# Optimization experiments

Hardware: AMD Instinct MI355X
Metric: run time of the kernel (lower is better)

Reference implementation:

```python
import jax, jax.numpy as jnp
import numpy as np

T, D = 4096, 2048
H, DK, DV = 6, 256, 512        # heads, head_k_dim, head_v_dim (expand_v=2)
KD, VD = H * DK, H * DV        # 1536, 3072
KSZ = 4                        # conv_size
GEN = D // 8                   # generator reduction 8 -> 256
EPS = 1e-5                     # norm_eps


def setup_inputs() -> dict:
    key = jax.random.key(0)
    ks = jax.random.split(key, 12)
    std = 0.02
    p = lambda i, shape: jax.random.normal(ks[i], shape, jnp.float32) * std
    rng = np.random.default_rng(0)
    A = rng.uniform(0.0, 16.0, H).astype(np.float32)
    dt = np.exp(rng.uniform(0, 1, H) * (np.log(0.1) - np.log(0.001)) + np.log(0.001)).astype(np.float32)
    dt = np.clip(dt, 1e-4, None)
    inv_dt = (dt + np.log(-np.expm1(-dt))).astype(np.float32)
    return {
        'hidden_states': jax.random.normal(ks[0], (T, D), jnp.float32),
        'Wq': p(1, (D, KD)), 'Wk': p(2, (D, KD)), 'Wv': p(3, (D, VD)),
        'Wb': p(4, (D, H)), 'Wa': p(5, (D, H)), 'Wg': p(6, (D, VD)), 'Wo': p(7, (VD, D)),
        'A_log': jnp.asarray(np.log(A)), 'dt_bias': jnp.asarray(inv_dt),
        'conv_w': p(8, (VD, KSZ)), 'gen_w1': p(9, (D, GEN)), 'gen_w2': p(10, (GEN, KSZ)),
        'norm_w': jnp.ones((DV,), jnp.float32),
    }


def _l2norm(x):
    return x * jax.lax.rsqrt(jnp.sum(x * x, -1, keepdims=True) + 1e-6)


def reference(hidden_states, Wq, Wk, Wv, Wb, Wa, Wg, Wo, A_log, dt_bias, conv_w, gen_w1, gen_w2, norm_w):
    h = hidden_states[None]                             # [1,T,D]
    q = jax.nn.silu(h @ Wq)                             # [1,T,KD]
    k = jax.nn.silu(h @ Wk)
    x = h @ Wv                                          # [1,T,VD]
    # dynamic short convolution: per-token kernel added to static depthwise kernel
    dyn = jax.nn.silu(h @ gen_w1) @ gen_w2              # [1,T,KSZ]
    xpad = jnp.pad(x, ((0, 0), (KSZ - 1, 0), (0, 0)))   # causal padding
    v = jnp.zeros_like(x)
    for j in range(KSZ):
        v = v + (conv_w[None, None, :, j] + dyn[:, :, None, j]) * xpad[:, j:j + x.shape[1], :]
    v = jax.nn.silu(v)

    B = 1
    q = _l2norm(q.reshape(B, -1, H, DK))                # use_qk_l2norm_in_kernel=True
    k = _l2norm(k.reshape(B, -1, H, DK))
    v = v.reshape(B, -1, H, DV)
    beta = jax.nn.sigmoid(h @ Wb)                       # [1,T,H]
    g = -jnp.exp(A_log) * jax.nn.softplus(h @ Wa + dt_bias)  # [1,T,H] decay log-gates
    scale = DK ** -0.5

    def step(S, inp):                                   # gated delta rule recurrence
        qt, kt, vt, gt, bt = inp
        S = S * jnp.exp(gt)[..., None, None]            # [B,H,DK,DV]
        dv = (vt - jnp.einsum('bhk,bhkv->bhv', kt, S)) * bt[..., None]
        S = S + kt[..., :, None] * dv[..., None, :]
        ot = jnp.einsum('bhk,bhkv->bhv', qt, S) * scale
        return S, ot

    S0 = jnp.zeros((B, H, DK, DV), jnp.float32)
    tm = lambda a: jnp.moveaxis(a, 1, 0)                # time-major for scan
    _, o = jax.lax.scan(step, S0, (tm(q), tm(k), tm(v), tm(g), tm(beta)))
    o = jnp.moveaxis(o, 0, 1)                           # [1,T,H,DV]

    gate = (h @ Wg).reshape(B, -1, H, DV)
    rms = jax.lax.rsqrt(jnp.mean(o * o, -1, keepdims=True) + EPS)
    o = o * rms * norm_w * jax.nn.silu(gate)            # gated RMSNorm
    o = o.reshape(B, -1, VD) @ Wo                       # [1,T,D]
    return o[0]
```

## Files before the change

### kernel.cpp

```cpp
#include <hip/hip_runtime.h>
#include <hip/hip_bf16.h>
#include <math.h>

#define T_LEN 4096
#define DIM   2048
#define NH    6
#define DK    256
#define DVh   512
#define KD    1536
#define VD    3072
#define CK    64
#define NCHK  (T_LEN / CK)

typedef __attribute__((ext_vector_type(8))) short bf16x8;
typedef __attribute__((ext_vector_type(4))) float f32x4;

__device__ __forceinline__ float silu_f(float v){ return v / (1.f + __expf(-v)); }

__device__ __forceinline__ unsigned short f2bf(float f) {
  unsigned int u = __float_as_uint(f);
  unsigned int r = u + 0x7FFFu + ((u >> 16) & 1u);
  return (unsigned short)(r >> 16);
}
__device__ __forceinline__ float bf2f(unsigned short s) {
  return __uint_as_float(((unsigned int)s) << 16);
}

__device__ __forceinline__ void bar_lds() {
  __builtin_amdgcn_sched_barrier(0);
  asm volatile("s_waitcnt lgkmcnt(0)" ::: "memory");
  __builtin_amdgcn_s_barrier();
  __builtin_amdgcn_sched_barrier(0);
}

__global__ __launch_bounds__(256) void cast_bf16(
    const float* __restrict__ in, unsigned short* __restrict__ out)
{
  int i = blockIdx.x * 256 + threadIdx.x;
  float4 v4 = ((const float4*)in)[i];
  ushort4 o4;
  o4.x = f2bf(v4.x); o4.y = f2bf(v4.y); o4.z = f2bf(v4.z); o4.w = f2bf(v4.w);
  ((ushort4*)out)[i] = o4;
}

__global__ __launch_bounds__(256) void tcast(
    const float* __restrict__ in, unsigned short* __restrict__ out, int R, int Cn)
{
  __shared__ float tile[32][33];
  int bx = blockIdx.x * 32;
  int by = blockIdx.y * 32;
  int tx = threadIdx.x & 31, ty = threadIdx.x >> 5;
#pragma unroll
  for (int i = 0; i < 32; i += 8)
    tile[ty + i][tx] = in[(size_t)(by + ty + i) * Cn + bx + tx];
  __syncthreads();
#pragma unroll
  for (int i = 0; i < 32; i += 8)
    out[(size_t)(bx + ty + i) * R + by + tx] = f2bf(tile[tx][ty + i]);
}

__global__ __launch_bounds__(256) void gemm_bt_bf16(
    const unsigned short* __restrict__ A, const unsigned short* __restrict__ BT,
    void* __restrict__ Cout, int M, int N, int K, int act)
{
  __shared__ unsigned short As[128 * 32];
  __shared__ unsigned short Bs[128 * 32];
  const int tid = threadIdx.x;
  const int bm = blockIdx.y * 128, bn = blockIdx.x * 128;
  const int lane = tid & 63, wave = tid >> 6;
  const int wm = (wave >> 1) * 64, wn = (wave & 1) * 64;
  const int fr = lane & 15, kq = lane >> 4;

  f32x4 acc[4][4];
#pragma unroll
  for (int i = 0; i < 4; ++i)
#pragma unroll
    for (int j = 0; j < 4; ++j) acc[i][j] = (f32x4){0.f, 0.f, 0.f, 0.f};

  const int r0 = tid >> 2, c0 = (tid & 3) * 8;
  const int r1 = r0 + 64;

  for (int k0 = 0; k0 < K; k0 += 32) {
    __builtin_amdgcn_global_load_lds(
        (const __attribute__((address_space(1))) unsigned int*)(A + (size_t)(bm + r0) * K + k0 + c0),
        (__attribute__((address_space(3))) unsigned int*)(As + r0 * 32 + c0), 16, 0, 0);
    __builtin_amdgcn_global_load_lds(
        (const __attribute__((address_space(1))) unsigned int*)(A + (size_t)(bm + r1) * K + k0 + c0),
        (__attribute__((address_space(3))) unsigned int*)(As + r1 * 32 + c0), 16, 0, 0);
    __builtin_amdgcn_global_load_lds(
        (const __attribute__((address_space(1))) unsigned int*)(BT + (size_t)(bn + r0) * K + k0 + c0),
        (__attribute__((address_space(3))) unsigned int*)(Bs + r0 * 32 + c0), 16, 0, 0);
    __builtin_amdgcn_global_load_lds(
        (const __attribute__((address_space(1))) unsigned int*)(BT + (size_t)(bn + r1) * K + k0 + c0),
        (__attribute__((address_space(3))) unsigned int*)(Bs + r1 * 32 + c0), 16, 0, 0);
    __syncthreads();

    bf16x8 af[4], bfr[4];
#pragma unroll
    for (int i = 0; i < 4; ++i)
      af[i] = *(const bf16x8*)(As + (wm + i * 16 + fr) * 32 + kq * 8);
#pragma unroll
    for (int j = 0; j < 4; ++j)
      bfr[j] = *(const bf16x8*)(Bs + (wn + j * 16 + fr) * 32 + kq * 8);
#pragma unroll
    for (int i = 0; i < 4; ++i)
#pragma unroll
      for (int j = 0; j < 4; ++j)
        acc[i][j] = __builtin_amdgcn_mfma_f32_16x16x32_bf16(af[i], bfr[j], acc[i][j], 0, 0, 0);
    __syncthreads();
  }

  if (act == 2) {
    unsigned short* C = (unsigned short*)Cout;
#pragma unroll
    for (int i = 0; i < 4; ++i) {
      int rbase = bm + wm + i * 16 + kq * 4;
#pragma unroll
      for (int r = 0; r < 4; ++r) {
        size_t rowoff = (size_t)(rbase + r) * N + bn + wn + fr;
#pragma unroll
        for (int j = 0; j < 4; ++j) C[rowoff + j * 16] = f2bf(acc[i][j][r]);
      }
    }
  } else {
    float* C = (float*)Cout;
#pragma unroll
    for (int i = 0; i < 4; ++i) {
      int rbase = bm + wm + i * 16 + kq * 4;
#pragma unroll
      for (int r = 0; r < 4; ++r) {
        size_t rowoff = (size_t)(rbase + r) * N + bn + wn + fr;
#pragma unroll
        for (int j = 0; j < 4; ++j) {
          float v = acc[i][j][r];
          if (act == 1) v = silu_f(v);
          C[rowoff + j * 16] = v;
        }
      }
    }
  }
}

__global__ __launch_bounds__(256) void proj_dyn(
    const float* __restrict__ tg, const float* __restrict__ w2, float* __restrict__ dyn)
{
  int t = blockIdx.x, tid = threadIdx.x;
  float g = tg[(size_t)t * 256 + tid];
  float p[4];
#pragma unroll
  for (int j = 0; j < 4; ++j) p[j] = g * w2[tid * 4 + j];
#pragma unroll
  for (int j = 0; j < 4; ++j)
    for (int m = 32; m >= 1; m >>= 1) p[j] += __shfl_xor(p[j], m);
  __shared__ float red[4][4];
  if ((tid & 63) == 0) {
    int w = tid >> 6;
#pragma unroll
    for (int j = 0; j < 4; ++j) red[w][j] = p[j];
  }
  __syncthreads();
  if (tid < 4) dyn[(size_t)t * 4 + tid] = red[0][tid] + red[1][tid] + red[2][tid] + red[3][tid];
}

__global__ __launch_bounds__(256) void proj_bg(
    const float* __restrict__ h, const float* __restrict__ Wb, const float* __restrict__ Wa,
    const float* __restrict__ A_log, const float* __restrict__ dt_bias,
    float* __restrict__ beta, float* __restrict__ gout)
{
  int t = blockIdx.x, tid = threadIdx.x;
  float pb[6], pa[6];
#pragma unroll
  for (int j = 0; j < 6; ++j) { pb[j] = 0.f; pa[j] = 0.f; }
  for (int d = tid; d < DIM; d += 256) {
    float hv = h[(size_t)t * DIM + d];
#pragma unroll
    for (int j = 0; j < 6; ++j) {
      pb[j] += hv * Wb[d * 6 + j];
      pa[j] += hv * Wa[d * 6 + j];
    }
  }
#pragma unroll
  for (int j = 0; j < 6; ++j)
    for (int m = 32; m >= 1; m >>= 1) { pb[j] += __shfl_xor(pb[j], m); pa[j] += __shfl_xor(pa[j], m); }
  __shared__ float rb[4][6], ra[4][6];
  if ((tid & 63) == 0) {
    int w = tid >> 6;
#pragma unroll
    for (int j = 0; j < 6; ++j) { rb[w][j] = pb[j]; ra[w][j] = pa[j]; }
  }
  __syncthreads();
  if (tid < 6) {
    int j = tid;
    float sb = rb[0][j] + rb[1][j] + rb[2][j] + rb[3][j];
    float sa = ra[0][j] + ra[1][j] + ra[2][j] + ra[3][j];
    beta[(size_t)t * 6 + j] = 1.f / (1.f + expf(-sb));
    float z = sa + dt_bias[j];
    float sp = (z > 20.f) ? z : log1pf(expf(z));
    gout[(size_t)t * 6 + j] = -expf(A_log[j]) * sp;
  }
}

__global__ __launch_bounds__(256) void conv_kernel(
    const float* __restrict__ x, const float* __restrict__ dyn,
    const float* __restrict__ cw, float* __restrict__ v)
{
  int c = blockIdx.x * 256 + threadIdx.x;
  int t = blockIdx.y;
  float4 w4 = ((const float4*)cw)[c];
  float d0 = dyn[t * 4 + 0], d1 = dyn[t * 4 + 1], d2 = dyn[t * 4 + 2], d3 = dyn[t * 4 + 3];
  float acc = (w4.w + d3) * x[(size_t)t * VD + c];
  if (t >= 1) acc += (w4.z + d2) * x[(size_t)(t - 1) * VD + c];
  if (t >= 2) acc += (w4.y + d1) * x[(size_t)(t - 2) * VD + c];
  if (t >= 3) acc += (w4.x + d0) * x[(size_t)(t - 3) * VD + c];
  v[(size_t)t * VD + c] = silu_f(acc);
}

__global__ __launch_bounds__(64) void l2norm_qk(
    float* __restrict__ q, float* __restrict__ k)
{
  size_t base = (size_t)blockIdx.x * 256;
  int tid = threadIdx.x;
  float4 qv = ((float4*)(q + base))[tid];
  float4 kv = ((float4*)(k + base))[tid];
  float sq = qv.x*qv.x + qv.y*qv.y + qv.z*qv.z + qv.w*qv.w;
  float sk = kv.x*kv.x + kv.y*kv.y + kv.z*kv.z + kv.w*kv.w;
  for (int m = 32; m >= 1; m >>= 1) { sq += __shfl_xor(sq, m); sk += __shfl_xor(sk, m); }
  float rq = rsqrtf(sq + 1e-6f) * 0.0625f;
  float rk = rsqrtf(sk + 1e-6f);
  qv.x *= rq; qv.y *= rq; qv.z *= rq; qv.w *= rq;
  kv.x *= rk; kv.y *= rk; kv.z *= rk; kv.w *= rk;
  ((float4*)(q + base))[tid] = qv;
  ((float4*)(k + base))[tid] = kv;
}

__global__ __launch_bounds__(64) void cumsum_g(
    const float* __restrict__ g, float* __restrict__ c, float* __restrict__ gammas)
{
  int ch = blockIdx.x, h = blockIdx.y;
  int t0 = ch * CK;
  int lane = threadIdx.x;
  float cum = g[(size_t)(t0 + lane) * 6 + h];
  for (int off = 1; off < 64; off <<= 1) {
    float n = __shfl_up(cum, off);
    if (lane >= off) cum += n;
  }
  c[(size_t)h * T_LEN + t0 + lane] = cum;
  if (lane == 63) gammas[h * NCHK + ch] = __expf(cum);
}

__global__ __launch_bounds__(384) void scale_kq(
    const float* __restrict__ q, const float* __restrict__ k, const float* __restrict__ c,
    unsigned short* __restrict__ Qb, unsigned short* __restrict__ Kb)
{
  int t = blockIdx.x;
  int tid = threadIdx.x;
  int h = tid >> 6;
  float w1 = __expf(c[(size_t)h * T_LEN + t]);
  size_t off = (size_t)t * KD + tid * 4;
  float4 qv = *(const float4*)(q + off);
  float4 kv = *(const float4*)(k + off);
  ushort4 qo, ko;
  qo.x = f2bf(w1 * qv.x); qo.y = f2bf(w1 * qv.y); qo.z = f2bf(w1 * qv.z); qo.w = f2bf(w1 * qv.w);
  ko.x = f2bf(w1 * kv.x); ko.y = f2bf(w1 * kv.y); ko.z = f2bf(w1 * kv.z); ko.w = f2bf(w1 * kv.w);
  *(ushort4*)(Qb + off) = qo;
  *(ushort4*)(Kb + off) = ko;
}

__global__ __launch_bounds__(256) void make_khT(
    const float* __restrict__ k, const float* __restrict__ c,
    unsigned short* __restrict__ KhT)
{
  int ch = blockIdx.x, h = blockIdx.y;
  int t0 = ch * CK;
  int tt = threadIdx.x & 63, ks = threadIdx.x >> 6;
  float cend = c[(size_t)h * T_LEN + t0 + 63];
  float w2 = __expf(cend - c[(size_t)h * T_LEN + t0 + tt]);
  size_t obase = ((size_t)(h * NCHK + ch)) * DK * CK;
#pragma unroll 8
  for (int kb2 = 0; kb2 < 64; ++kb2) {
    int kk = ks * 64 + kb2;
    float kv = k[(size_t)(t0 + tt) * KD + h * 256 + kk];
    KhT[obase + (size_t)kk * CK + tt] = f2bf(w2 * kv);
  }
}

__global__ __launch_bounds__(256) void chunk_lp(
    const float* __restrict__ q, const float* __restrict__ k,
    const float* __restrict__ c, const float* __restrict__ beta,
    float* __restrict__ Lg, unsigned short* __restrict__ Pm)
{
  const int ch = blockIdx.x, h = blockIdx.y;
  const int t0 = ch * CK;
  const int tid = threadIdx.x;
  const int w = tid >> 6, lane = tid & 63, fr = lane & 15, kq = lane >> 4;
  __shared__ unsigned short kb[64][264];
  __shared__ unsigned short qb[64][264];
  __shared__ float cs[64], bs[64];
#pragma unroll
  for (int i = 0; i < 16; ++i) {
    int fi = tid + i * 256;
    int r = fi >> 6, d4 = fi & 63;
    float4 kv = *(const float4*)(k + (size_t)(t0 + r) * KD + h * 256 + d4 * 4);
    float4 qv = *(const float4*)(q + (size_t)(t0 + r) * KD + h * 256 + d4 * 4);
    ushort4 k4, q4;
    k4.x = f2bf(kv.x); k4.y = f2bf(kv.y); k4.z = f2bf(kv.z); k4.w = f2bf(kv.w);
    q4.x = f2bf(qv.x); q4.y = f2bf(qv.y); q4.z = f2bf(qv.z); q4.w = f2bf(qv.w);
    *(ushort4*)&kb[r][d4 * 4] = k4;
    *(ushort4*)&qb[r][d4 * 4] = q4;
  }
  if (tid < 64) {
    cs[tid] = c[(size_t)h * T_LEN + t0 + tid];
    bs[tid] = beta[(size_t)(t0 + tid) * 6 + h];
  }
  __syncthreads();

  f32x4 akk[4], aqk[4];
#pragma unroll
  for (int j = 0; j < 4; ++j) { akk[j] = (f32x4){0,0,0,0}; aqk[j] = (f32x4){0,0,0,0}; }
#pragma unroll
  for (int kt = 0; kt < 8; ++kt) {
    bf16x8 ak = *(const bf16x8*)&kb[16 * w + fr][kt * 32 + kq * 8];
    bf16x8 aq = *(const bf16x8*)&qb[16 * w + fr][kt * 32 + kq * 8];
#pragma unroll
    for (int j = 0; j < 4; ++j) {
      bf16x8 b = *(const bf16x8*)&kb[j * 16 + fr][kt * 32 + kq * 8];
      akk[j] = __builtin_amdgcn_mfma_f32_16x16x32_bf16(ak, b, akk[j], 0, 0, 0);
      aqk[j] = __builtin_amdgcn_mfma_f32_16x16x32_bf16(aq, b, aqk[j], 0, 0, 0);
    }
  }
  size_t base = ((size_t)(h * NCHK + ch)) * CK * CK;
#pragma unroll
  for (int j = 0; j < 4; ++j) {
#pragma unroll
    for (int r = 0; r < 4; ++r) {
      int t = 16 * w + kq * 4 + r, col = j * 16 + fr;
      float e = __expf(fminf(cs[t] - cs[col], 0.f));
      Lg[base + t * 64 + col] = (col < t) ? bs[t] * e * akk[j][r] : 0.f;
      Pm[base + t * 64 + col] = f2bf((col <= t) ? e * aqk[j][r] : 0.f);
    }
  }
}

__global__ __launch_bounds__(64) void tri_inv(
    const float* __restrict__ Lg, const float* __restrict__ beta,
    unsigned short* __restrict__ Tm)
{
  const int ch = blockIdx.x, h = blockIdx.y;
  const size_t base = ((size_t)(h * NCHK + ch)) * CK * CK;
  const int j = threadIdx.x;
  __shared__ float Ll[64][65];
  __shared__ float Tl[64][65];
  for (int t = 0; t < 64; ++t) Ll[t][j] = Lg[base + t * 64 + j];
  __syncthreads();
  for (int t = 0; t < 64; ++t) {
    float s;
    if (j > t) s = 0.f;
    else if (j == t) s = 1.f;
    else {
      s = 0.f;
      for (int m = j; m < t; ++m) s -= Ll[t][m] * Tl[m][j];
    }
    Tl[t][j] = s;
  }
  float bj = beta[(size_t)(ch * 64 + j) * 6 + h];
  for (int t = 0; t < 64; ++t) Tm[base + t * 64 + j] = f2bf(Tl[t][j] * bj);
}

__global__ __launch_bounds__(256) void scan_chunk(
    const unsigned short* __restrict__ Kb,
    const unsigned short* __restrict__ Qb,
    const unsigned short* __restrict__ KhT,
    const unsigned short* __restrict__ Tm,
    const unsigned short* __restrict__ Pm,
    const float* __restrict__ gammas,
    float* __restrict__ VO)
{
  const int h = blockIdx.y, sl = blockIdx.x;
  const int tid = threadIdx.x;
  const int w = tid >> 6, lane = tid & 63;
  const int fr = lane & 15, kq = lane >> 4;

  __shared__ unsigned short S0h[16][264];
  __shared__ unsigned short S0l[16][264];
  __shared__ unsigned short XT[16][72];
  __shared__ unsigned short DVT[16][72];

  f32x4 st[4];
#pragma unroll
  for (int i = 0; i < 4; ++i) st[i] = (f32x4){0.f, 0.f, 0.f, 0.f};

  const int colg = h * DVh + sl * 16 + fr;
  const size_t hc0 = (size_t)h * NCHK;

  bf16x8 kfA[8], kfB[8];
  float vlA[4], vlB[4];

#define PREF_KV(KF, VL, chn) do { \
    const unsigned short* krow_ = Kb + (size_t)((chn) * CK + 16 * w + fr) * KD + h * 256 + kq * 8; \
    _Pragma("unroll") \
    for (int kt = 0; kt < 8; ++kt) KF[kt] = *(const bf16x8*)(krow_ + kt * 32); \
    _Pragma("unroll") \
    for (int r = 0; r < 4; ++r) VL[r] = VO[(size_t)((chn) * CK + 16 * w + kq * 4 + r) * VD + colg]; \
  } while (0)

#define CHUNK_BODY(chx, KF, VL, KFN, VLN) do { \
    const int ch_ = (chx); \
    const int t0_ = ch_ * CK; \
    const size_t cb_ = hc0 + ch_; \
     \
    bf16x8 qf[8]; \
    { const unsigned short* qrow_ = Qb + (size_t)(t0_ + 16 * w + fr) * KD + h * 256 + kq * 8; \
      _Pragma("unroll") \
      for (int kt = 0; kt < 8; ++kt) qf[kt] = *(const bf16x8*)(qrow_ + kt * 32); } \
    bf16x8 tf[2], pf[2]; \
    { const unsigned short* trow_ = Tm + (cb_ * CK + 16 * w + fr) * CK + kq * 8; \
      const unsigned short* prow_ = Pm + (cb_ * CK + 16 * w + fr) * CK + kq * 8; \
      tf[0] = *(const bf16x8*)(trow_); tf[1] = *(const bf16x8*)(trow_ + 32); \
      pf[0] = *(const bf16x8*)(prow_); pf[1] = *(const bf16x8*)(prow_ + 32); } \
    bf16x8 hfr[4][2]; \
    _Pragma("unroll") \
    for (int i = 0; i < 4; ++i) { \
      const unsigned short* hrow_ = KhT + (cb_ * DK + 64 * w + 16 * i + fr) * CK + kq * 8; \
      hfr[i][0] = *(const bf16x8*)(hrow_); hfr[i][1] = *(const bf16x8*)(hrow_ + 32); } \
    const float gam_ = gammas[cb_]; \
     \
    _Pragma("unroll") \
    for (int i = 0; i < 4; ++i) { \
      ushort4 hi4, lo4; \
      float s0 = st[i][0], s1 = st[i][1], s2 = st[i][2], s3 = st[i][3]; \
      hi4.x = f2bf(s0); lo4.x = f2bf(s0 - bf2f(hi4.x)); \
      hi4.y = f2bf(s1); lo4.y = f2bf(s1 - bf2f(hi4.y)); \
      hi4.z = f2bf(s2); lo4.z = f2bf(s2 - bf2f(hi4.z)); \
      hi4.w = f2bf(s3); lo4.w = f2bf(s3 - bf2f(hi4.w)); \
      *(ushort4*)&S0h[fr][64 * w + 16 * i + kq * 4] = hi4; \
      *(ushort4*)&S0l[fr][64 * w + 16 * i + kq * 4] = lo4; } \
     \
    { const int chn_ = (ch_ + 1 < NCHK) ? ch_ + 1 : ch_; PREF_KV(KFN, VLN, chn_); } \
    bar_lds(); \
     \
    { f32x4 yh = (f32x4){0.f,0.f,0.f,0.f}, yl = (f32x4){0.f,0.f,0.f,0.f}; \
      _Pragma("unroll") \
      for (int kt = 0; kt < 8; ++kt) { \
        bf16x8 bh_ = *(const bf16x8*)&S0h[fr][kt * 32 + kq * 8]; \
        bf16x8 bl_ = *(const bf16x8*)&S0l[fr][kt * 32 + kq * 8]; \
        yh = __builtin_amdgcn_mfma_f32_16x16x32_bf16(KF[kt], bh_, yh, 0, 0, 0); \
        yl = __builtin_amdgcn_mfma_f32_16x16x32_bf16(KF[kt], bl_, yl, 0, 0, 0); } \
      ushort4 x4; \
      x4.x = f2bf(VL[0] - (yh[0] + yl[0])); \
      x4.y = f2bf(VL[1] - (yh[1] + yl[1])); \
      x4.z = f2bf(VL[2] - (yh[2] + yl[2])); \
      x4.w = f2bf(VL[3] - (yh[3] + yl[3])); \
      *(ushort4*)&XT[fr][16 * w + kq * 4] = x4; } \
    bar_lds(); \
     \
    { f32x4 d = (f32x4){0.f,0.f,0.f,0.f}; \
      _Pragma("unroll") \
      for (int kt = 0; kt < 2; ++kt) { \
        bf16x8 b_ = *(const bf16x8*)&XT[fr][kt * 32 + kq * 8]; \
        d = __builtin_amdgcn_mfma_f32_16x16x32_bf16(tf[kt], b_, d, 0, 0, 0); } \
      ushort4 d4; \
      d4.x = f2bf(d[0]); d4.y = f2bf(d[1]); d4.z = f2bf(d[2]); d4.w = f2bf(d[3]); \
      *(ushort4*)&DVT[fr][16 * w + kq * 4] = d4; } \
    bar_lds(); \
     \
    { f32x4 oh = (f32x4){0.f,0.f,0.f,0.f}, ol = (f32x4){0.f,0.f,0.f,0.f}, op = (f32x4){0.f,0.f,0.f,0.f}; \
      _Pragma("unroll") \
      for (int kt = 0; kt < 8; ++kt) { \
        bf16x8 bh_ = *(const bf16x8*)&S0h[fr][kt * 32 + kq * 8]; \
        bf16x8 bl_ = *(const bf16x8*)&S0l[fr][kt * 32 + kq * 8]; \
        oh = __builtin_amdgcn_mfma_f32_16x16x32_bf16(qf[kt], bh_, oh, 0, 0, 0); \
        ol = __builtin_amdgcn_mfma_f32_16x16x32_bf16(qf[kt], bl_, ol, 0, 0, 0); } \
      _Pragma("unroll") \
      for (int kt = 0; kt < 2; ++kt) { \
        bf16x8 b_ = *(const bf16x8*)&DVT[fr][kt * 32 + kq * 8]; \
        op = __builtin_amdgcn_mfma_f32_16x16x32_bf16(pf[kt], b_, op, 0, 0, 0); } \
      _Pragma("unroll") \
      for (int r = 0; r < 4; ++r) \
        VO[(size_t)(t0_ + 16 * w + kq * 4 + r) * VD + colg] = oh[r] + ol[r] + op[r]; } \
     \
    _Pragma("unroll") \
    for (int i = 0; i < 4; ++i) { \
      st[i][0] *= gam_; st[i][1] *= gam_; st[i][2] *= gam_; st[i][3] *= gam_; \
      _Pragma("unroll") \
      for (int kt = 0; kt < 2; ++kt) { \
        bf16x8 b_ = *(const bf16x8*)&DVT[fr][kt * 32 + kq * 8]; \
        st[i] = __builtin_amdgcn_mfma_f32_16x16x32_bf16(hfr[i][kt], b_, st[i], 0, 0, 0); } } \
    bar_lds(); \
  } while (0)

  PREF_KV(kfA, vlA, 0);
  for (int ch = 0; ch < NCHK; ch += 2) {
    CHUNK_BODY(ch,     kfA, vlA, kfB, vlB);
    CHUNK_BODY(ch + 1, kfB, vlB, kfA, vlA);
  }
#undef CHUNK_BODY
#undef PREF_KV
}

__global__ __launch_bounds__(256) void norm_gate(
    const float* __restrict__ o, const unsigned short* __restrict__ gate,
    const float* __restrict__ nw, unsigned short* __restrict__ out)
{
  int th = blockIdx.x, tid = threadIdx.x;
  size_t base = (size_t)th * DVh;
  float x0 = o[base + tid], x1 = o[base + 256 + tid];
  float ss = x0 * x0 + x1 * x1;
  for (int m = 32; m >= 1; m >>= 1) ss += __shfl_xor(ss, m);
  __shared__ float red[4];
  if ((tid & 63) == 0) red[tid >> 6] = ss;
  __syncthreads();
  float rms = rsqrtf((red[0] + red[1] + red[2] + red[3]) * (1.f / 512.f) + 1e-5f);
  float g0 = bf2f(gate[base + tid]), g1 = bf2f(gate[base + 256 + tid]);
  out[base + tid]       = f2bf(x0 * rms * nw[tid]       * silu_f(g0));
  out[base + 256 + tid] = f2bf(x1 * rms * nw[tid + 256] * silu_f(g1));
}

extern "C" void kernel_launch(void* const* d_in, const int* in_sizes, int n_in,
                              void* d_out, int out_size, void* d_ws, size_t ws_size,
                              hipStream_t stream)
{
  const float* h       = (const float*)d_in[0];
  const float* Wq      = (const float*)d_in[1];
  const float* Wk      = (const float*)d_in[2];
  const float* Wv      = (const float*)d_in[3];
  const float* Wb      = (const float*)d_in[4];
  const float* Wa      = (const float*)d_in[5];
  const float* Wg      = (const float*)d_in[6];
  const float* Wo      = (const float*)d_in[7];
  const float* A_log   = (const float*)d_in[8];
  const float* dt_bias = (const float*)d_in[9];
  const float* conv_w  = (const float*)d_in[10];
  const float* gen_w1  = (const float*)d_in[11];
  const float* gen_w2  = (const float*)d_in[12];
  const float* norm_w  = (const float*)d_in[13];
  float* out = (float*)d_out;

  const size_t TK = (size_t)T_LEN * KD, TV = (size_t)T_LEN * VD, TD = (size_t)T_LEN * DIM;

  float* ws   = (float*)d_ws;
  float* q    = ws;
  float* k    = q    + TK;
  float* x    = k    + TK;
  float* v    = x    + TV;
  float* tg   = v    + TV;
  float* dyn  = tg   + (size_t)T_LEN * 256;
  float* beta = dyn  + (size_t)T_LEN * 4;
  float* g    = beta + (size_t)T_LEN * 6;
  float* c    = g    + (size_t)T_LEN * 6;
  float* gam  = c    + (size_t)NH * T_LEN;
  float* fend = gam  + 512;
  unsigned short* bh      = (unsigned short*)fend;
  unsigned short* wT      = bh      + TD;
  unsigned short* gate_bf = wT      + (size_t)DIM * VD;
  unsigned short* go_bf   = gate_bf + TV;
  unsigned short* Kb_s  = bh;
  unsigned short* Qb_s  = (unsigned short*)x;
  unsigned short* KhT_s = Qb_s + TK;
  unsigned short* Tm_s  = KhT_s + TK;
  unsigned short* Pm_s  = Tm_s + (size_t)NH * NCHK * CK * CK;
  float* Lg = (float*)go_bf;

  dim3 blk(256);
  cast_bf16<<<(TD / 4) / 256, blk, 0, stream>>>(h, bh);
  tcast<<<dim3(KD / 32, DIM / 32), blk, 0, stream>>>(Wq, wT, DIM, KD);
  gemm_bt_bf16<<<dim3(KD / 128, T_LEN / 128), blk, 0, stream>>>(bh, wT, q, T_LEN, KD, DIM, 1);
  tcast<<<dim3(KD / 32, DIM / 32), blk, 0, stream>>>(Wk, wT, DIM, KD);
  gemm_bt_bf16<<<dim3(KD / 128, T_LEN / 128), blk, 0, stream>>>(bh, wT, k, T_LEN, KD, DIM, 1);
  tcast<<<dim3(VD / 32, DIM / 32), blk, 0, stream>>>(Wv, wT, DIM, VD);
  gemm_bt_bf16<<<dim3(VD / 128, T_LEN / 128), blk, 0, stream>>>(bh, wT, x, T_LEN, VD, DIM, 0);
  tcast<<<dim3(VD / 32, DIM / 32), blk, 0, stream>>>(Wg, wT, DIM, VD);
  gemm_bt_bf16<<<dim3(VD / 128, T_LEN / 128), blk, 0, stream>>>(bh, wT, gate_bf, T_LEN, VD, DIM, 2);
  tcast<<<dim3(256 / 32, DIM / 32), blk, 0, stream>>>(gen_w1, wT, DIM, 256);
  gemm_bt_bf16<<<dim3(256 / 128, T_LEN / 128), blk, 0, stream>>>(bh, wT, tg, T_LEN, 256, DIM, 1);

  proj_dyn<<<T_LEN, blk, 0, stream>>>(tg, gen_w2, dyn);
  proj_bg<<<T_LEN, blk, 0, stream>>>(h, Wb, Wa, A_log, dt_bias, beta, g);
  conv_kernel<<<dim3(VD / 256, T_LEN), blk, 0, stream>>>(x, dyn, conv_w, v);
  l2norm_qk<<<T_LEN * NH, 64, 0, stream>>>(q, k);

  cumsum_g<<<dim3(NCHK, NH), 64, 0, stream>>>(g, c, gam);
  scale_kq<<<T_LEN, 384, 0, stream>>>(q, k, c, Qb_s, Kb_s);
  make_khT<<<dim3(NCHK, NH), blk, 0, stream>>>(k, c, KhT_s);
  chunk_lp<<<dim3(NCHK, NH), blk, 0, stream>>>(q, k, c, beta, Lg, Pm_s);
  tri_inv<<<dim3(NCHK, NH), 64, 0, stream>>>(Lg, beta, Tm_s);

  scan_chunk<<<dim3(DVh / 16, NH), blk, 0, stream>>>(Kb_s, Qb_s, KhT_s, Tm_s, Pm_s, gam, v);

  norm_gate<<<T_LEN * NH, blk, 0, stream>>>(v, gate_bf, norm_w, go_bf);
  tcast<<<dim3(DIM / 32, VD / 32), blk, 0, stream>>>(Wo, wT, VD, DIM);
  gemm_bt_bf16<<<dim3(DIM / 128, T_LEN / 128), blk, 0, stream>>>(go_bf, wT, out, T_LEN, DIM, VD, 0);
}
```

Baseline: 1.074 ms.

## Restructure chunk recurrence to cut barriers and prefetch Q with K

```diff
diff --git a/kernel.cpp b/kernel.cpp
--- a/kernel.cpp
+++ b/kernel.cpp
@@ -392,26 +392,35 @@
   const int colg = h * DVh + sl * 16 + fr;
   const size_t hc0 = (size_t)h * NCHK;
 
-  bf16x8 kfA[8], kfB[8];
+  {
+    int zr = tid >> 4;
+    int zc = (tid & 15) * 16;
+    ushort4 z; z.x = 0; z.y = 0; z.z = 0; z.w = 0;
+#pragma unroll
+    for (int u = 0; u < 4; ++u) {
+      *(ushort4*)&S0h[zr][zc + 4 * u] = z;
+      *(ushort4*)&S0l[zr][zc + 4 * u] = z;
+    }
+  }
+
+  bf16x8 kfA[8], kfB[8], qfA[8], qfB[8];
   float vlA[4], vlB[4];
 
-#define PREF_KV(KF, VL, chn) do { \
+#define PREF_KQV(KF, QF, VL, chn) do { \
     const unsigned short* krow_ = Kb + (size_t)((chn) * CK + 16 * w + fr) * KD + h * 256 + kq * 8; \
+    const unsigned short* qrow_ = Qb + (size_t)((chn) * CK + 16 * w + fr) * KD + h * 256 + kq * 8; \
     _Pragma("unroll") \
-    for (int kt = 0; kt < 8; ++kt) KF[kt] = *(const bf16x8*)(krow_ + kt * 32); \
+    for (int kt = 0; kt < 8; ++kt) { \
+      KF[kt] = *(const bf16x8*)(krow_ + kt * 32); \
+      QF[kt] = *(const bf16x8*)(qrow_ + kt * 32); } \
     _Pragma("unroll") \
     for (int r = 0; r < 4; ++r) VL[r] = VO[(size_t)((chn) * CK + 16 * w + kq * 4 + r) * VD + colg]; \
   } while (0)
 
-#define CHUNK_BODY(chx, KF, VL, KFN, VLN) do { \
+#define CHUNK_BODY(chx, KF, QF, VL, KFN, QFN, VLN) do { \
     const int ch_ = (chx); \
     const int t0_ = ch_ * CK; \
     const size_t cb_ = hc0 + ch_; \
-     \
-    bf16x8 qf[8]; \
-    { const unsigned short* qrow_ = Qb + (size_t)(t0_ + 16 * w + fr) * KD + h * 256 + kq * 8; \
-      _Pragma("unroll") \
-      for (int kt = 0; kt < 8; ++kt) qf[kt] = *(const bf16x8*)(qrow_ + kt * 32); } \
     bf16x8 tf[2], pf[2]; \
     { const unsigned short* trow_ = Tm + (cb_ * CK + 16 * w + fr) * CK + kq * 8; \
       const unsigned short* prow_ = Pm + (cb_ * CK + 16 * w + fr) * CK + kq * 8; \
@@ -424,27 +433,19 @@
       hfr[i][0] = *(const bf16x8*)(hrow_); hfr[i][1] = *(const bf16x8*)(hrow_ + 32); } \
     const float gam_ = gammas[cb_]; \
      \
-    _Pragma("unroll") \
-    for (int i = 0; i < 4; ++i) { \
-      ushort4 hi4, lo4; \
-      float s0 = st[i][0], s1 = st[i][1], s2 = st[i][2], s3 = st[i][3]; \
-      hi4.x = f2bf(s0); lo4.x = f2bf(s0 - bf2f(hi4.x)); \
-      hi4.y = f2bf(s1); lo4.y = f2bf(s1 - bf2f(hi4.y)); \
-      hi4.z = f2bf(s2); lo4.z = f2bf(s2 - bf2f(hi4.z)); \
-      hi4.w = f2bf(s3); lo4.w = f2bf(s3 - bf2f(hi4.w)); \
-      *(ushort4*)&S0h[fr][64 * w + 16 * i + kq * 4] = hi4; \
-      *(ushort4*)&S0l[fr][64 * w + 16 * i + kq * 4] = lo4; } \
+    { const int chn_ = (ch_ + 1 < NCHK) ? ch_ + 1 : ch_; PREF_KQV(KFN, QFN, VLN, chn_); } \
      \
-    { const int chn_ = (ch_ + 1 < NCHK) ? ch_ + 1 : ch_; PREF_KV(KFN, VLN, chn_); } \
-    bar_lds(); \
      \
+    f32x4 oh = (f32x4){0.f,0.f,0.f,0.f}, ol = (f32x4){0.f,0.f,0.f,0.f}; \
     { f32x4 yh = (f32x4){0.f,0.f,0.f,0.f}, yl = (f32x4){0.f,0.f,0.f,0.f}; \
       _Pragma("unroll") \
       for (int kt = 0; kt < 8; ++kt) { \
         bf16x8 bh_ = *(const bf16x8*)&S0h[fr][kt * 32 + kq * 8]; \
         bf16x8 bl_ = *(const bf16x8*)&S0l[fr][kt * 32 + kq * 8]; \
         yh = __builtin_amdgcn_mfma_f32_16x16x32_bf16(KF[kt], bh_, yh, 0, 0, 0); \
-        yl = __builtin_amdgcn_mfma_f32_16x16x32_bf16(KF[kt], bl_, yl, 0, 0, 0); } \
+        yl = __builtin_amdgcn_mfma_f32_16x16x32_bf16(KF[kt], bl_, yl, 0, 0, 0); \
+        oh = __builtin_amdgcn_mfma_f32_16x16x32_bf16(QF[kt], bh_, oh, 0, 0, 0); \
+        ol = __builtin_amdgcn_mfma_f32_16x16x32_bf16(QF[kt], bl_, ol, 0, 0, 0); } \
       ushort4 x4; \
       x4.x = f2bf(VL[0] - (yh[0] + yl[0])); \
       x4.y = f2bf(VL[1] - (yh[1] + yl[1])); \
@@ -454,47 +455,48 @@
     bar_lds(); \
      \
     { f32x4 d = (f32x4){0.f,0.f,0.f,0.f}; \
-      _Pragma("unroll") \
-      for (int kt = 0; kt < 2; ++kt) { \
-        bf16x8 b_ = *(const bf16x8*)&XT[fr][kt * 32 + kq * 8]; \
-        d = __builtin_amdgcn_mfma_f32_16x16x32_bf16(tf[kt], b_, d, 0, 0, 0); } \
+      bf16x8 b0_ = *(const bf16x8*)&XT[fr][kq * 8]; \
+      bf16x8 b1_ = *(const bf16x8*)&XT[fr][32 + kq * 8]; \
+      d = __builtin_amdgcn_mfma_f32_16x16x32_bf16(tf[0], b0_, d, 0, 0, 0); \
+      d = __builtin_amdgcn_mfma_f32_16x16x32_bf16(tf[1], b1_, d, 0, 0, 0); \
       ushort4 d4; \
       d4.x = f2bf(d[0]); d4.y = f2bf(d[1]); d4.z = f2bf(d[2]); d4.w = f2bf(d[3]); \
       *(ushort4*)&DVT[fr][16 * w + kq * 4] = d4; } \
     bar_lds(); \
      \
-    { f32x4 oh = (f32x4){0.f,0.f,0.f,0.f}, ol = (f32x4){0.f,0.f,0.f,0.f}, op = (f32x4){0.f,0.f,0.f,0.f}; \
-      _Pragma("unroll") \
-      for (int kt = 0; kt < 8; ++kt) { \
-        bf16x8 bh_ = *(const bf16x8*)&S0h[fr][kt * 32 + kq * 8]; \
-        bf16x8 bl_ = *(const bf16x8*)&S0l[fr][kt * 32 + kq * 8]; \
-        oh = __builtin_amdgcn_mfma_f32_16x16x32_bf16(qf[kt], bh_, oh, 0, 0, 0); \
-        ol = __builtin_amdgcn_mfma_f32_16x16x32_bf16(qf[kt], bl_, ol, 0, 0, 0); } \
-      _Pragma("unroll") \
-      for (int kt = 0; kt < 2; ++kt) { \
-        bf16x8 b_ = *(const bf16x8*)&DVT[fr][kt * 32 + kq * 8]; \
-        op = __builtin_amdgcn_mfma_f32_16x16x32_bf16(pf[kt], b_, op, 0, 0, 0); } \
+     \
+    { bf16x8 dv0_ = *(const bf16x8*)&DVT[fr][kq * 8]; \
+      bf16x8 dv1_ = *(const bf16x8*)&DVT[fr][32 + kq * 8]; \
+      f32x4 op = (f32x4){0.f,0.f,0.f,0.f}; \
+      op = __builtin_amdgcn_mfma_f32_16x16x32_bf16(pf[0], dv0_, op, 0, 0, 0); \
+      op = __builtin_amdgcn_mfma_f32_16x16x32_bf16(pf[1], dv1_, op, 0, 0, 0); \
       _Pragma("unroll") \
       for (int r = 0; r < 4; ++r) \
-        VO[(size_t)(t0_ + 16 * w + kq * 4 + r) * VD + colg] = oh[r] + ol[r] + op[r]; } \
-     \
-    _Pragma("unroll") \
-    for (int i = 0; i < 4; ++i) { \
-      st[i][0] *= gam_; st[i][1] *= gam_; st[i][2] *= gam_; st[i][3] *= gam_; \
+        VO[(size_t)(t0_ + 16 * w + kq * 4 + r) * VD + colg] = oh[r] + ol[r] + op[r]; \
       _Pragma("unroll") \
-      for (int kt = 0; kt < 2; ++kt) { \
-        bf16x8 b_ = *(const bf16x8*)&DVT[fr][kt * 32 + kq * 8]; \
-        st[i] = __builtin_amdgcn_mfma_f32_16x16x32_bf16(hfr[i][kt], b_, st[i], 0, 0, 0); } } \
+      for (int i = 0; i < 4; ++i) { \
+        st[i][0] *= gam_; st[i][1] *= gam_; st[i][2] *= gam_; st[i][3] *= gam_; \
+        st[i] = __builtin_amdgcn_mfma_f32_16x16x32_bf16(hfr[i][0], dv0_, st[i], 0, 0, 0); \
+        st[i] = __builtin_amdgcn_mfma_f32_16x16x32_bf16(hfr[i][1], dv1_, st[i], 0, 0, 0); \
+        ushort4 hi4, lo4; \
+        { float s0 = st[i][0], s1 = st[i][1], s2 = st[i][2], s3 = st[i][3]; \
+          hi4.x = f2bf(s0); lo4.x = f2bf(s0 - bf2f(hi4.x)); \
+          hi4.y = f2bf(s1); lo4.y = f2bf(s1 - bf2f(hi4.y)); \
+          hi4.z = f2bf(s2); lo4.z = f2bf(s2 - bf2f(hi4.z)); \
+          hi4.w = f2bf(s3); lo4.w = f2bf(s3 - bf2f(hi4.w)); } \
+        *(ushort4*)&S0h[fr][64 * w + 16 * i + kq * 4] = hi4; \
+        *(ushort4*)&S0l[fr][64 * w + 16 * i + kq * 4] = lo4; } } \
     bar_lds(); \
   } while (0)
 
-  PREF_KV(kfA, vlA, 0);
+  PREF_KQV(kfA, qfA, vlA, 0);
+  __syncthreads();
   for (int ch = 0; ch < NCHK; ch += 2) {
-    CHUNK_BODY(ch,     kfA, vlA, kfB, vlB);
-    CHUNK_BODY(ch + 1, kfB, vlB, kfA, vlA);
+    CHUNK_BODY(ch,     kfA, qfA, vlA, kfB, qfB, vlB);
+    CHUNK_BODY(ch + 1, kfB, qfB, vlB, kfA, qfA, vlA);
   }
 #undef CHUNK_BODY
-#undef PREF_KV
+#undef PREF_KQV
 }
 
 __global__ __launch_bounds__(256) void norm_gate(
```

Result: faster. 1.050 ms (-2.3%).
